# Kernel tuning notes

Hardware: AMD Instinct MI355X
Metric: run time of the kernel (lower is better)

Reference implementation:

```python
import jax, jax.numpy as jnp
import numpy as np

WIN = (4, 4, 4)   # (wd, wh, ww), window seq len s = 64
HEADS = 4


def setup_inputs() -> dict:
    key = jax.random.key(0)
    k1, k2, k3 = jax.random.split(key, 3)
    B, D, H, W, C = 1, 32, 64, 128, 96
    x = jax.random.normal(k1, (B, D, H, W, C), dtype=jnp.float32)
    # weights stored in (in, out) layout; math identical to torch Linear (x @ W.T)
    w_qkv = jax.random.normal(k2, (C, 3 * C), dtype=jnp.float32) * (C ** -0.5)
    w_proj = jax.random.normal(k3, (C, C), dtype=jnp.float32) * (C ** -0.5)
    b_proj = jnp.zeros((C,), dtype=jnp.float32)
    return {"x": x, "w_qkv": w_qkv, "w_proj": w_proj, "b_proj": b_proj}


def reference(x, w_qkv, w_proj, b_proj):
    B, D, H, W, C = x.shape
    wd, wh, ww = WIN
    h = HEADS
    ch = C // h
    s = wd * wh * ww
    scale = ch ** -0.5
    n, m, l = D // wd, H // wh, W // ww
    # window partition: [B,D,H,W,C] -> [B,n,m,l,s,C]
    xw = x.reshape(B, n, wd, m, wh, l, ww, C)
    xw = xw.transpose(0, 1, 3, 5, 2, 4, 6, 7).reshape(B, n, m, l, s, C)
    # QKV projection (no bias)
    qkv = xw @ w_qkv                      # [B,n,m,l,s,3C]
    q, k, v = jnp.split(qkv, 3, axis=-1)  # each [B,n,m,l,s,C]

    def to_heads(t):
        return t.reshape(B, n, m, l, s, h, ch).transpose(0, 1, 2, 3, 5, 4, 6)

    q, k, v = to_heads(q), to_heads(k), to_heads(v)  # [B,n,m,l,h,s,ch]
    attn = jnp.einsum('bnmlhsc,bnmlhtc->bnmlhst', q, k) * scale
    attn = jax.nn.softmax(attn, axis=-1)             # [B,n,m,l,h,s,s]
    out = jnp.einsum('bnmlhst,bnmlhtc->bnmlhsc', attn, v)
    # merge heads: [B,n,m,l,h,s,ch] -> [B,n,m,l,s,C]
    out = out.transpose(0, 1, 2, 3, 5, 4, 6).reshape(B, n, m, l, s, C)
    out = out @ w_proj + b_proj
    # window merge back to [B,D,H,W,C]
    out = out.reshape(B, n, m, l, wd, wh, ww, C)
    out = out.transpose(0, 1, 4, 2, 5, 3, 6, 7).reshape(B, D, H, W, C)
    return out
```

## Files before the change

### kernel.cpp

```cpp
#include <hip/hip_runtime.h>
#include <hip/hip_bf16.h>

typedef __attribute__((ext_vector_type(8))) short bf16x8;
typedef __attribute__((ext_vector_type(4))) float f32x4;
typedef __attribute__((ext_vector_type(4))) unsigned short u16x4;
typedef __attribute__((ext_vector_type(4))) unsigned int u32x4;

#define MFMA16(a, b, c) __builtin_amdgcn_mfma_f32_16x16x32_bf16((a), (b), (c), 0, 0, 0)

#define WQT_ELEMS 27648
#define WPT_ELEMS 9216

__device__ __forceinline__ unsigned short f2bf(float f) {
    union { float f; unsigned u; } v; v.f = f;
    return (unsigned short)((v.u + 0x7FFFu + ((v.u >> 16) & 1u)) >> 16);
}
__device__ __forceinline__ unsigned pack2bf(float a, float b) {
    return (unsigned)f2bf(a) | ((unsigned)f2bf(b) << 16);
}

__global__ void wconv_kernel(const float* __restrict__ wqkv,
                             const float* __restrict__ wproj,
                             unsigned short* __restrict__ wsT) {
    int o = blockIdx.x * 256 + threadIdx.x;
    if (o < WQT_ELEMS) {
        int j = o / 96, c = o % 96;
        wsT[o] = f2bf(wqkv[c * 288 + j]);
    } else if (o < WQT_ELEMS + WPT_ELEMS) {
        int o2 = o - WQT_ELEMS;
        int j = o2 / 96, c = o2 % 96;
        wsT[o] = f2bf(wproj[c * 96 + j]);
    }
}

__global__ __launch_bounds__(256, 3)
void winattn_kernel(const float* __restrict__ x,
                    const unsigned short* __restrict__ wsT,
                    const float* __restrict__ bproj,
                    float* __restrict__ out) {
    __shared__ __align__(16) unsigned short xs[64 * 96];
    __shared__ __align__(16) unsigned short qs[64 * 96 + 8];
    __shared__ __align__(16) unsigned short ks[64 * 128];
    __shared__ __align__(16) unsigned short vt[96 * 64];

    char* ksb = (char*)ks;
    char* vtb = (char*)vt;

    const int tid = threadIdx.x;
    const int lane = tid & 63;
    const int wv = tid >> 6;
    const int p  = lane & 15;
    const int qg = lane >> 4;

    const int iw  = blockIdx.x;
    const int l_i = iw & 31;
    const int m_i = (iw >> 5) & 15;
    const int n_i = iw >> 9;

    const f32x4 fzero = {0.f, 0.f, 0.f, 0.f};
    const float qscale = 0.2944889313f;

    #pragma unroll
    for (int it = 0; it < 6; ++it) {
        int slot = tid + it * 256;
        int t = slot / 24, cq = slot % 24;
        int td = t >> 4, th = (t >> 2) & 3, tw = t & 3;
        int off = (((n_i * 4 + td) * 64 + (m_i * 4 + th)) * 128 + (l_i * 4 + tw)) * 96 + cq * 4;
        float4 v4 = *reinterpret_cast<const float4*>(x + off);
        u16x4 h;
        h[0] = f2bf(v4.x); h[1] = f2bf(v4.y); h[2] = f2bf(v4.z); h[3] = f2bf(v4.w);
        *reinterpret_cast<u16x4*>(&xs[t * 96 + cq * 4]) = h;
    }
    {
        int t = tid >> 2, hd = tid & 3;
        bf16x8 z = {0, 0, 0, 0, 0, 0, 0, 0};
        int cb = hd * 64 + 48;
        *reinterpret_cast<bf16x8*>(ksb + t * 256 + (cb ^ ((t & 7) << 4))) = z;
    }
    if (tid < 8) qs[64 * 96 + tid] = 0;
    __syncthreads();

    bf16x8 afr[4][3];
    #pragma unroll
    for (int mt = 0; mt < 4; ++mt)
        #pragma unroll
        for (int kt = 0; kt < 3; ++kt)
            afr[mt][kt] = *reinterpret_cast<const bf16x8*>(&xs[(mt * 16 + p) * 96 + kt * 32 + qg * 8]);

    auto do_tile = [&](int nt) {
        f32x4 acc[4] = {fzero, fzero, fzero, fzero};
        #pragma unroll
        for (int kt = 0; kt < 3; ++kt) {
            bf16x8 bfr = *reinterpret_cast<const bf16x8*>(&wsT[(nt * 16 + p) * 96 + kt * 32 + qg * 8]);
            #pragma unroll
            for (int mt = 0; mt < 4; ++mt)
                acc[mt] = MFMA16(afr[mt][kt], bfr, acc[mt]);
        }
        int jcol = nt * 16 + p;
        if (jcol < 96) {
            #pragma unroll
            for (int mt = 0; mt < 4; ++mt)
                #pragma unroll
                for (int rg = 0; rg < 4; ++rg)
                    qs[(mt * 16 + qg * 4 + rg) * 96 + jcol] = f2bf(acc[mt][rg] * qscale);
        } else if (jcol < 192) {
            int jk = jcol - 96;
            int hd = jk / 24, kk = jk % 24;
            int cb = hd * 64 + kk * 2;
            #pragma unroll
            for (int mt = 0; mt < 4; ++mt)
                #pragma unroll
                for (int rg = 0; rg < 4; ++rg) {
                    int t = mt * 16 + qg * 4 + rg;
                    *reinterpret_cast<unsigned short*>(ksb + t * 256 + (cb ^ ((t & 7) << 4))) = f2bf(acc[mt][rg]);
                }
        } else {
            int jv = jcol - 192;
            int hd = jv / 24, cc = jv % 24;
            int vr = hd * 24 + cc;
            int rb = vr * 128, sw = (vr & 7) << 4;
            #pragma unroll
            for (int mt = 0; mt < 4; ++mt)
                #pragma unroll
                for (int rg = 0; rg < 4; ++rg) {
                    int u = mt * 16 + qg * 4 + rg;
                    *reinterpret_cast<unsigned short*>(vtb + rb + ((u * 2) ^ sw)) = f2bf(acc[mt][rg]);
                }
        }
    };
    int base = (wv < 2) ? wv * 5 : 10 + (wv - 2) * 4;
    #pragma unroll
    for (int i = 0; i < 4; ++i) do_tile(base + i);
    if (wv < 2) do_tile(base + 4);
    __syncthreads();

    #pragma unroll 1
    for (int hd = 0; hd < 4; ++hd) {
        bf16x8 aqh = *reinterpret_cast<const bf16x8*>(&qs[(wv * 16 + p) * 96 + hd * 24 + qg * 8]);
        f32x4 sacc[4];
        #pragma unroll
        for (int nt = 0; nt < 4; ++nt) {
            int t = nt * 16 + p;
            bf16x8 ak = *reinterpret_cast<const bf16x8*>(ksb + t * 256 + ((hd * 64 + qg * 16) ^ ((t & 7) << 4)));
            sacc[nt] = MFMA16(ak, aqh, fzero);
        }
        float mm = sacc[0][0];
        #pragma unroll
        for (int nt = 0; nt < 4; ++nt)
            #pragma unroll
            for (int rg = 0; rg < 4; ++rg)
                mm = fmaxf(mm, sacc[nt][rg]);
        mm = fmaxf(mm, __shfl_xor(mm, 16));
        mm = fmaxf(mm, __shfl_xor(mm, 32));
        float pw[4][4];
        float sum = 0.f;
        #pragma unroll
        for (int nt = 0; nt < 4; ++nt)
            #pragma unroll
            for (int rg = 0; rg < 4; ++rg) {
                float e = exp2f(sacc[nt][rg] - mm);
                pw[nt][rg] = e;
                sum += e;
            }
        sum += __shfl_xor(sum, 16);
        sum += __shfl_xor(sum, 32);
        float inv = 1.0f / sum;
        unsigned pk[4][2];
        #pragma unroll
        for (int nt = 0; nt < 4; ++nt) {
            pk[nt][0] = pack2bf(pw[nt][0] * inv, pw[nt][1] * inv);
            pk[nt][1] = pack2bf(pw[nt][2] * inv, pw[nt][3] * inv);
        }
        u32x4 pa0, pa1;
        #pragma unroll
        for (int d = 0; d < 4; ++d) {
            int src = ((qg & 1) * 2 + (d >> 1)) * 16 + p;
            int lo0 = __shfl((int)pk[0][d & 1], src);
            int hi0 = __shfl((int)pk[1][d & 1], src);
            int lo1 = __shfl((int)pk[2][d & 1], src);
            int hi1 = __shfl((int)pk[3][d & 1], src);
            pa0[d] = (qg < 2) ? (unsigned)lo0 : (unsigned)hi0;
            pa1[d] = (qg < 2) ? (unsigned)lo1 : (unsigned)hi1;
        }
        bf16x8 a0 = __builtin_bit_cast(bf16x8, pa0);
        bf16x8 a1 = __builtin_bit_cast(bf16x8, pa1);
        f32x4 oacc[2] = {fzero, fzero};
        #pragma unroll
        for (int n2 = 0; n2 < 2; ++n2) {
            int vr = hd * 24 + n2 * 16 + p;
            vr = vr > 95 ? 95 : vr;
            int rb = vr * 128, sw = (vr & 7) << 4;
            bf16x8 bv0 = *reinterpret_cast<const bf16x8*>(vtb + rb + ((qg * 16) ^ sw));
            bf16x8 bv1 = *reinterpret_cast<const bf16x8*>(vtb + rb + ((64 + qg * 16) ^ sw));
            oacc[n2] = MFMA16(a0, bv0, oacc[n2]);
            oacc[n2] = MFMA16(a1, bv1, oacc[n2]);
        }
        #pragma unroll
        for (int n2 = 0; n2 < 2; ++n2) {
            int cc = n2 * 16 + p;
            if (cc < 24) {
                #pragma unroll
                for (int rg = 0; rg < 4; ++rg)
                    xs[(wv * 16 + qg * 4 + rg) * 96 + hd * 24 + cc] = f2bf(oacc[n2][rg]);
            }
        }
    }

    bf16x8 ofr[3];
    #pragma unroll
    for (int kt = 0; kt < 3; ++kt)
        ofr[kt] = *reinterpret_cast<const bf16x8*>(&xs[(wv * 16 + p) * 96 + kt * 32 + qg * 8]);
    const unsigned short* wpT = wsT + WQT_ELEMS;
    int obase = (((n_i * 4 + wv) * 64 + (m_i * 4 + qg)) * 128 + l_i * 4) * 96;
    #pragma unroll
    for (int nt = 0; nt < 6; ++nt) {
        f32x4 acc = fzero;
        #pragma unroll
        for (int kt = 0; kt < 3; ++kt) {
            bf16x8 bfr = *reinterpret_cast<const bf16x8*>(&wpT[(nt * 16 + p) * 96 + kt * 32 + qg * 8]);
            acc = MFMA16(ofr[kt], bfr, acc);
        }
        float bias = bproj[nt * 16 + p];
        #pragma unroll
        for (int rg = 0; rg < 4; ++rg)
            out[obase + rg * 96 + nt * 16 + p] = acc[rg] + bias;
    }
}

extern "C" void kernel_launch(void* const* d_in, const int* in_sizes, int n_in,
                              void* d_out, int out_size, void* d_ws, size_t ws_size,
                              hipStream_t stream) {
    const float* x     = (const float*)d_in[0];
    const float* wqkv  = (const float*)d_in[1];
    const float* wproj = (const float*)d_in[2];
    const float* bproj = (const float*)d_in[3];
    float* out = (float*)d_out;
    unsigned short* wsT = (unsigned short*)d_ws;

    wconv_kernel<<<dim3((WQT_ELEMS + WPT_ELEMS) / 256), dim3(256), 0, stream>>>(wqkv, wproj, wsT);
    winattn_kernel<<<dim3(4096), dim3(256), 0, stream>>>(x, wsT, bproj, out);
}
```

Before: 87.86 us.

## Merge x and Q LDS buffers with swizzle, fold q-scale into weights, raise occupancy

The x tile and the Q tile now share one swizzled LDS buffer, so LDS per block drops from about 52KB to 40KB. This lets the launch bounds rise to 4 blocks per CU, and an extra barrier is added so x fragments are read before Q overwrites them. The attention scale is folded into the Q columns of the bf16 weight conversion, and the hand-written bf16 rounding is replaced with the library conversion. The costs are an extra sync and XOR address arithmetic, plus possible register pressure from the higher occupancy target.

```diff
diff --git a/kernel.cpp b/kernel.cpp
--- a/kernel.cpp
+++ b/kernel.cpp
@@ -11,12 +11,12 @@
 #define WQT_ELEMS 27648
 #define WPT_ELEMS 9216
 
-__device__ __forceinline__ unsigned short f2bf(float f) {
-    union { float f; unsigned u; } v; v.f = f;
-    return (unsigned short)((v.u + 0x7FFFu + ((v.u >> 16) & 1u)) >> 16);
+__device__ __forceinline__ unsigned short cvt_bf(float f) {
+    __hip_bfloat16 h = __float2bfloat16(f);
+    return *reinterpret_cast<unsigned short*>(&h);
 }
 __device__ __forceinline__ unsigned pack2bf(float a, float b) {
-    return (unsigned)f2bf(a) | ((unsigned)f2bf(b) << 16);
+    return (unsigned)cvt_bf(a) | ((unsigned)cvt_bf(b) << 16);
 }
 
 __global__ void wconv_kernel(const float* __restrict__ wqkv,
@@ -25,26 +25,29 @@
     int o = blockIdx.x * 256 + threadIdx.x;
     if (o < WQT_ELEMS) {
         int j = o / 96, c = o % 96;
-        wsT[o] = f2bf(wqkv[c * 288 + j]);
+        float w = wqkv[c * 288 + j];
+        if (j < 96) w *= 0.2944889313f;
+        wsT[o] = cvt_bf(w);
     } else if (o < WQT_ELEMS + WPT_ELEMS) {
         int o2 = o - WQT_ELEMS;
         int j = o2 / 96, c = o2 % 96;
-        wsT[o] = f2bf(wproj[c * 96 + j]);
-    }
-}
-
-__global__ __launch_bounds__(256, 3)
+        wsT[o] = cvt_bf(wproj[c * 96 + j]);
+    }
+}
+
+__device__ __forceinline__ int xq_addr(int t, int c) {
+    return ((c >> 5) << 12) + ((t >> 1) << 7)
+         + ((((t & 1) << 6) + ((c & 31) << 1)) ^ (((t >> 1) & 7) << 4));
+}
+
+__global__ __launch_bounds__(256, 4)
 void winattn_kernel(const float* __restrict__ x,
                     const unsigned short* __restrict__ wsT,
                     const float* __restrict__ bproj,
                     float* __restrict__ out) {
-    __shared__ __align__(16) unsigned short xs[64 * 96];
-    __shared__ __align__(16) unsigned short qs[64 * 96 + 8];
-    __shared__ __align__(16) unsigned short ks[64 * 128];
-    __shared__ __align__(16) unsigned short vt[96 * 64];
-
-    char* ksb = (char*)ks;
-    char* vtb = (char*)vt;
+    __shared__ __align__(16) char xq[12288];
+    __shared__ __align__(16) char ksb[16384];
+    __shared__ __align__(16) char vtb[12288];
 
     const int tid = threadIdx.x;
     const int lane = tid & 63;
@@ -58,7 +61,6 @@
     const int n_i = iw >> 9;
 
     const f32x4 fzero = {0.f, 0.f, 0.f, 0.f};
-    const float qscale = 0.2944889313f;
 
     #pragma unroll
     for (int it = 0; it < 6; ++it) {
@@ -68,8 +70,8 @@
         int off = (((n_i * 4 + td) * 64 + (m_i * 4 + th)) * 128 + (l_i * 4 + tw)) * 96 + cq * 4;
         float4 v4 = *reinterpret_cast<const float4*>(x + off);
         u16x4 h;
-        h[0] = f2bf(v4.x); h[1] = f2bf(v4.y); h[2] = f2bf(v4.z); h[3] = f2bf(v4.w);
-        *reinterpret_cast<u16x4*>(&xs[t * 96 + cq * 4]) = h;
+        h[0] = cvt_bf(v4.x); h[1] = cvt_bf(v4.y); h[2] = cvt_bf(v4.z); h[3] = cvt_bf(v4.w);
+        *reinterpret_cast<u16x4*>(xq + xq_addr(t, cq * 4)) = h;
     }
     {
         int t = tid >> 2, hd = tid & 3;
@@ -77,7 +79,6 @@
         int cb = hd * 64 + 48;
         *reinterpret_cast<bf16x8*>(ksb + t * 256 + (cb ^ ((t & 7) << 4))) = z;
     }
-    if (tid < 8) qs[64 * 96 + tid] = 0;
     __syncthreads();
 
     bf16x8 afr[4][3];
@@ -85,7 +86,8 @@
     for (int mt = 0; mt < 4; ++mt)
         #pragma unroll
         for (int kt = 0; kt < 3; ++kt)
-            afr[mt][kt] = *reinterpret_cast<const bf16x8*>(&xs[(mt * 16 + p) * 96 + kt * 32 + qg * 8]);
+            afr[mt][kt] = *reinterpret_cast<const bf16x8*>(xq + xq_addr(mt * 16 + p, kt * 32 + qg * 8));
+    __syncthreads();
 
     auto do_tile = [&](int nt) {
         f32x4 acc[4] = {fzero, fzero, fzero, fzero};
@@ -102,7 +104,7 @@
             for (int mt = 0; mt < 4; ++mt)
                 #pragma unroll
                 for (int rg = 0; rg < 4; ++rg)
-                    qs[(mt * 16 + qg * 4 + rg) * 96 + jcol] = f2bf(acc[mt][rg] * qscale);
+                    *reinterpret_cast<unsigned short*>(xq + xq_addr(mt * 16 + qg * 4 + rg, jcol)) = cvt_bf(acc[mt][rg]);
         } else if (jcol < 192) {
             int jk = jcol - 96;
             int hd = jk / 24, kk = jk % 24;
@@ -112,7 +114,7 @@
                 #pragma unroll
                 for (int rg = 0; rg < 4; ++rg) {
                     int t = mt * 16 + qg * 4 + rg;
-                    *reinterpret_cast<unsigned short*>(ksb + t * 256 + (cb ^ ((t & 7) << 4))) = f2bf(acc[mt][rg]);
+                    *reinterpret_cast<unsigned short*>(ksb + t * 256 + (cb ^ ((t & 7) << 4))) = cvt_bf(acc[mt][rg]);
                 }
         } else {
             int jv = jcol - 192;
@@ -124,7 +126,7 @@
                 #pragma unroll
                 for (int rg = 0; rg < 4; ++rg) {
                     int u = mt * 16 + qg * 4 + rg;
-                    *reinterpret_cast<unsigned short*>(vtb + rb + ((u * 2) ^ sw)) = f2bf(acc[mt][rg]);
+                    *reinterpret_cast<unsigned short*>(vtb + rb + ((u * 2) ^ sw)) = cvt_bf(acc[mt][rg]);
                 }
         }
     };
@@ -136,7 +138,7 @@
 
     #pragma unroll 1
     for (int hd = 0; hd < 4; ++hd) {
-        bf16x8 aqh = *reinterpret_cast<const bf16x8*>(&qs[(wv * 16 + p) * 96 + hd * 24 + qg * 8]);
+        bf16x8 aqh = *reinterpret_cast<const bf16x8*>(xq + xq_addr(wv * 16 + p, hd * 24 + qg * 8));
         f32x4 sacc[4];
         #pragma unroll
         for (int nt = 0; nt < 4; ++nt) {
@@ -201,7 +203,7 @@
             if (cc < 24) {
                 #pragma unroll
                 for (int rg = 0; rg < 4; ++rg)
-                    xs[(wv * 16 + qg * 4 + rg) * 96 + hd * 24 + cc] = f2bf(oacc[n2][rg]);
+                    *reinterpret_cast<unsigned short*>(xq + xq_addr(wv * 16 + qg * 4 + rg, hd * 24 + cc)) = cvt_bf(oacc[n2][rg]);
             }
         }
     }
@@ -209,7 +211,7 @@
     bf16x8 ofr[3];
     #pragma unroll
     for (int kt = 0; kt < 3; ++kt)
-        ofr[kt] = *reinterpret_cast<const bf16x8*>(&xs[(wv * 16 + p) * 96 + kt * 32 + qg * 8]);
+        ofr[kt] = *reinterpret_cast<const bf16x8*>(xq + xq_addr(wv * 16 + p, kt * 32 + qg * 8));
     const unsigned short* wpT = wsT + WQT_ELEMS;
     int obase = (((n_i * 4 + wv) * 64 + (m_i * 4 + qg)) * 128 + l_i * 4) * 96;
     #pragma unroll
```

After: 107.8 us. 22.7% more time.
